# Performance work log

Hardware: AMD Instinct MI355X
Metric: run time of the kernel (lower is better)

## Reference

```python
import jax, jax.numpy as jnp
import numpy as np

D_MODEL = 768
N_HEADS = 12
HEAD_DIM = D_MODEL // N_HEADS


def setup_inputs() -> dict:
    key = jax.random.key(0)
    k_x, k_wqkv, k_bqkv, k_wp, k_bp = jax.random.split(key, 5)
    s = 1.0 / np.sqrt(D_MODEL)
    return {
        "x": jax.random.normal(k_x, (8, 1024, D_MODEL), dtype=jnp.float32),
        "w_qkv": jax.random.uniform(k_wqkv, (D_MODEL, 3 * D_MODEL), jnp.float32, -s, s),
        "b_qkv": jax.random.uniform(k_bqkv, (3 * D_MODEL,), jnp.float32, -s, s),
        "w_proj": jax.random.uniform(k_wp, (D_MODEL, D_MODEL), jnp.float32, -s, s),
        "b_proj": jax.random.uniform(k_bp, (D_MODEL,), jnp.float32, -s, s),
    }


def reference(x, w_qkv, b_qkv, w_proj, b_proj):
    # x: [B, N, D]. Dropout is identity in eval mode.
    B, N, D = x.shape
    qkv = x @ w_qkv + b_qkv  # [B, N, 3D]
    qkv = qkv.reshape(B, N, 3, N_HEADS, HEAD_DIM).transpose(2, 0, 3, 1, 4)
    q, k, v = qkv[0], qkv[1], qkv[2]  # each [B, H, N, hd]
    scale = 1.0 / np.sqrt(HEAD_DIM).astype(np.float32)
    attn = jnp.einsum("bhqd,bhkd->bhqk", q, k) * scale  # [B, H, N, N]
    attn = jax.nn.softmax(attn, axis=-1)
    out = jnp.einsum("bhqk,bhkd->bhqd", attn, v)  # [B, H, N, hd]
    out = out.transpose(0, 2, 1, 3).reshape(B, N, D)
    return out @ w_proj + b_proj
```

## Files before the change

kernel.cpp:

```cpp
#include <hip/hip_runtime.h>
#include <math.h>

#define D_MODEL 768
#define NHEADS  12
#define HDIM    64
#define SEQ     1024
#define BATCH   8
#define NBH     (BATCH*NHEADS)
#define M_TOTAL (BATCH*SEQ)
#define KT_D    (D_MODEL/32)
#define QKV_COLS (3*D_MODEL)

typedef __attribute__((ext_vector_type(8))) short bf16x8;
typedef __attribute__((ext_vector_type(4))) float f32x4;

#define MFMA16(a,b,c) __builtin_amdgcn_mfma_f32_16x16x32_bf16((a),(b),(c),0,0,0)

#define QSCALE 0.18033688011112042f

__device__ inline unsigned short f2bf(float f) {
    unsigned u = __float_as_uint(f);
    u += 0x7FFFu + ((u >> 16) & 1u);
    return (unsigned short)(u >> 16);
}
__device__ inline float bf2f(unsigned short h) {
    return __uint_as_float(((unsigned)h) << 16);
}
__device__ inline void gload16(const void* g, const void* l) {
    __builtin_amdgcn_global_load_lds(
        (const __attribute__((address_space(1))) unsigned*)g,
        (__attribute__((address_space(3))) unsigned*)l, 16, 0, 0);
}
__device__ inline float exp2_fast(float x) {
#if __has_builtin(__builtin_amdgcn_exp2f)
    return __builtin_amdgcn_exp2f(x);
#else
    float r; asm("v_exp_f32 %0, %1" : "=v"(r) : "v"(x)); return r;
#endif
}


#define NA_TOT 786432
#define NB1_TOT 221184
#define NB2_TOT 73728

__global__ __launch_bounds__(256)
void convert_all(const float* __restrict__ x,    unsigned short* __restrict__ Xf,
                 const float* __restrict__ wq,   unsigned short* __restrict__ Wq,
                 const float* __restrict__ wp,   unsigned short* __restrict__ Wp)
{
    const int gid = blockIdx.x * 256 + threadIdx.x;
    const int lane = gid & 63;
    if (gid < NA_TOT) {
        const int sub = gid >> 6;
        const int kt = sub % KT_D;
        const int mt = sub / KT_D;
        const float* s = x + (size_t)(mt*16 + (lane & 15)) * D_MODEL + kt*32 + (lane >> 4)*8;
        float4 v0 = *(const float4*)(s);
        float4 v1 = *(const float4*)(s + 4);
        float vv[8] = {v0.x, v0.y, v0.z, v0.w, v1.x, v1.y, v1.z, v1.w};
        union { unsigned short u[8]; bf16x8 v; } H;
        #pragma unroll
        for (int i = 0; i < 8; ++i) H.u[i] = f2bf(vv[i]);
        *(bf16x8*)(Xf + (size_t)sub * 512 + lane * 8) = H.v;
    } else {
        const float* src;
        unsigned short* dst;
        int sub, ldN;
        if (gid < NA_TOT + NB1_TOT) {
            src = wq; dst = Wq; ldN = QKV_COLS; sub = (gid - NA_TOT) >> 6;
        } else if (gid < NA_TOT + NB1_TOT + NB2_TOT) {
            src = wp; dst = Wp; ldN = D_MODEL; sub = (gid - NA_TOT - NB1_TOT) >> 6;
        } else {
            return;
        }
        const int kt = sub % KT_D;
        const int nt = sub / KT_D;
        const int n  = nt*16 + (lane & 15);
        const int k0 = kt*32 + (lane >> 4)*8;
        const float* s = src + (size_t)k0 * ldN + n;
        union { unsigned short u[8]; bf16x8 v; } H;
        #pragma unroll
        for (int i = 0; i < 8; ++i) H.u[i] = f2bf(s[(size_t)i * ldN]);
        *(bf16x8*)(dst + (size_t)sub * 512 + lane * 8) = H.v;
    }
}

template<int MODE>
__global__ __launch_bounds__(MODE == 0 ? 512 : 256, 4)
void gemm_frag(const unsigned short* __restrict__ Af,
               const unsigned short* __restrict__ Bf,
               const float* __restrict__ bias,
               float* __restrict__ outF,
               unsigned short* __restrict__ outQ,
               unsigned short* __restrict__ outK,
               unsigned short* __restrict__ outV)
{
    constexpr int NW     = (MODE == 0) ? 8 : 4;
    constexpr int NSUB_N = (MODE == 0) ? 8 : 4;
    constexpr int ACH    = 8;
    constexpr int NCH    = ACH + NSUB_N;
    constexpr int CPW    = NCH / NW;
    __shared__ unsigned short sm[3][NCH * 512];
    const int t = threadIdx.x, lane = t & 63, wid = t >> 6;
    const int wr = (MODE == 0) ? (wid >> 2) : (wid >> 1);
    const int wc = (MODE == 0) ? (wid & 3)  : (wid & 1);
    const int bid = blockIdx.x;
    const int mb = (bid & 7) * 8 + ((bid >> 3) & 7);
    const int nb = bid >> 6;

    auto stage = [&](int b, int ktv) {
        #pragma unroll
        for (int i = 0; i < CPW; ++i) {
            const int c = wid * CPW + i;
            const unsigned short* g;
            if (c < ACH) {
                g = Af + ((size_t)(mb*8 + c)*KT_D + ktv)*512 + lane*8;
            } else {
                const int j = c - ACH;
                g = Bf + ((size_t)(nb*NSUB_N + j)*KT_D + ktv)*512 + lane*8;
            }
            gload16(g, (const char*)&sm[b][0] + (size_t)c*1024);
        }
    };

    f32x4 acc[4][2] = {};

    stage(0, 0);
    stage(1, 1);

    for (int kt = 0; kt < KT_D; ++kt) {
        if (kt + 1 < KT_D) {
            if (MODE == 0) asm volatile("s_waitcnt vmcnt(2)" ::: "memory");
            else           asm volatile("s_waitcnt vmcnt(3)" ::: "memory");
        } else {
            asm volatile("s_waitcnt vmcnt(0)" ::: "memory");
        }
        __builtin_amdgcn_s_barrier();

        if (kt + 2 < KT_D) stage((kt + 2) % 3, kt + 2);

        const unsigned short* Lb = &sm[kt % 3][0];
        bf16x8 bh[2];
        #pragma unroll
        for (int n = 0; n < 2; ++n)
            bh[n] = *(const bf16x8*)(Lb + (ACH + wc*2 + n)*512 + lane*8);
        bf16x8 ah[4];
        #pragma unroll
        for (int m = 0; m < 4; ++m)
            ah[m] = *(const bf16x8*)(Lb + (wr*4 + m)*512 + lane*8);
        __builtin_amdgcn_s_setprio(1);
        #pragma unroll
        for (int m = 0; m < 4; ++m)
            #pragma unroll
            for (int n = 0; n < 2; ++n)
                acc[m][n] = MFMA16(ah[m], bh[n], acc[m][n]);
        __builtin_amdgcn_s_setprio(0);
    }

    const int rowW = mb*128 + wr*64;
    const int colW = nb*(NSUB_N*16) + wc*32;
    if (MODE == 1) {
        #pragma unroll
        for (int m = 0; m < 4; ++m)
            #pragma unroll
            for (int n = 0; n < 2; ++n) {
                const int col = colW + n*16 + (lane & 15);
                const float bv = bias[col];
                #pragma unroll
                for (int r = 0; r < 4; ++r) {
                    const int row = rowW + m*16 + (lane >> 4)*4 + r;
                    outF[(size_t)row * D_MODEL + col] = acc[m][n][r] + bv;
                }
            }
    } else {
        const int which = colW / D_MODEL;
        const int h     = (colW % D_MODEL) >> 6;
        #pragma unroll
        for (int m = 0; m < 4; ++m)
            #pragma unroll
            for (int n = 0; n < 2; ++n) {
                const int col = colW + n*16 + (lane & 15);
                const int d = col & 63;
                const float bv = bias[col];
                #pragma unroll
                for (int r = 0; r < 4; ++r) {
                    const int row = rowW + m*16 + (lane >> 4)*4 + r;
                    const int b = row >> 10, sq = row & 1023;
                    float val = acc[m][n][r] + bv;
                    if (which <= 1) {
                        if (which == 0) val *= QSCALE;
                        const int sub = (sq >> 4)*2 + (d >> 5);
                        const int lp  = (sq & 15) + (((d & 31) >> 3) << 4);
                        unsigned short* dst = (which == 0) ? outQ : outK;
                        dst[(size_t)(b*NHEADS + h)*65536
                            + (size_t)sub*512 + lp*8 + (d & 7)] = f2bf(val);
                    } else {
                        const int sub = (d >> 4)*32 + (sq >> 5);
                        const int lp  = (d & 15) + (((sq & 31) >> 3) << 4);
                        outV[(size_t)(b*NHEADS + h)*65536
                             + (size_t)sub*512 + lp*8 + (sq & 7)] = f2bf(val);
                    }
                }
            }
    }
}

__global__ __launch_bounds__(512, 6)
void attn_frag(const unsigned short* __restrict__ Qf,
               const unsigned short* __restrict__ Kf,
               const unsigned short* __restrict__ Vf,
               unsigned short* __restrict__ Cf)
{
    __shared__ unsigned short Ksm[2][8 * 512];
    __shared__ unsigned short Vsm[2][8 * 512];
    __shared__ unsigned short Psm[8 * 1024];

    const int t = threadIdx.x, lane = t & 63, wid = t >> 6;
    const int bid = blockIdx.x;
    const int qb  = (bid >> 3) & 7;
    const int bh  = (bid & 7) * 12 + (bid >> 6);
    const int mt0 = qb*8 + wid;
    const size_t kBase = (size_t)bh * 65536;

    const int slot  = lane & 7;
    const int colg  = (lane & 15) >> 3;
    const int qrow0 = (lane >> 4) * 4;

    auto stage = [&](int b, int jt) {
        #pragma unroll
        for (int i = 0; i < 2; ++i) {
            const int ch = wid*2 + i;
            if (ch < 8) {
                const unsigned short* gk = Kf + kBase + (size_t)(jt*8 + ch)*512;
                gload16(gk + lane*8, (const char*)&Ksm[b][0] + (size_t)ch*1024);
            } else {
                const int cv = ch - 8;
                const unsigned short* gv = Vf + kBase
                    + (size_t)((cv >> 1)*32 + jt*2 + (cv & 1))*512;
                gload16(gv + lane*8, (const char*)&Vsm[b][0] + (size_t)cv*1024);
            }
        }
    };

    stage(0, 0);

    bf16x8 qh[2];
    #pragma unroll
    for (int kt = 0; kt < 2; ++kt)
        qh[kt] = *(const bf16x8*)(Qf + kBase + ((size_t)mt0*2 + kt)*512 + lane*8);

    bf16x8 ones;
    #pragma unroll
    for (int i = 0; i < 8; ++i) ones[i] = (short)0x3F80;

    f32x4 out[4] = {};
    f32x4 lacc = {};
    float m_run[4];
    #pragma unroll
    for (int r = 0; r < 4; ++r) m_run[r] = -INFINITY;

    unsigned short* Pw = Psm + wid * 1024;

    __syncthreads();

    for (int jt = 0; jt < 16; ++jt) {
        const int cur = jt & 1;
        if (jt + 1 < 16) stage(cur ^ 1, jt + 1);

        f32x4 s[4] = {};
        __builtin_amdgcn_s_setprio(1);
        #pragma unroll
        for (int jn = 0; jn < 4; ++jn)
            #pragma unroll
            for (int kt = 0; kt < 2; ++kt) {
                const bf16x8 kh = *(const bf16x8*)(&Ksm[cur][0] + (jn*2 + kt)*512 + lane*8);
                s[jn] = MFMA16(qh[kt], kh, s[jn]);
            }
        __builtin_amdgcn_s_setprio(0);

        float mx[4];
        int ok = 1;
        #pragma unroll
        for (int r = 0; r < 4; ++r) {
            const float v = fmaxf(fmaxf(s[0][r], s[1][r]), fmaxf(s[2][r], s[3][r]));
            mx[r] = v;
            ok &= (v <= m_run[r] + 8.0f);
        }
        if (!__all(ok)) {
            float alf[4];
            #pragma unroll
            for (int r = 0; r < 4; ++r) {
                float v = mx[r];
                #pragma unroll
                for (int msk = 1; msk < 16; msk <<= 1)
                    v = fmaxf(v, __shfl_xor(v, msk));
                const float mn = fmaxf(m_run[r], v);
                alf[r] = exp2_fast(m_run[r] - mn);
                m_run[r] = mn;
            }
            #pragma unroll
            for (int dt = 0; dt < 4; ++dt)
                #pragma unroll
                for (int r = 0; r < 4; ++r)
                    out[dt][r] *= alf[r];
            #pragma unroll
            for (int r = 0; r < 4; ++r)
                lacc[r] *= alf[r];
        }

        #pragma unroll
        for (int r = 0; r < 4; ++r) {
            const float mb_ = m_run[r];
            const int tl   = qrow0 + r + (colg << 4);
            const int idxb = ((tl << 3) | slot) ^ (tl & 0x18);
            #pragma unroll
            for (int jn = 0; jn < 4; ++jn) {
                const float e = exp2_fast(s[jn][r] - mb_);
                Pw[(jn >> 1)*512 + idxb + ((jn & 1) << 8)]
                    = (unsigned short)(__float_as_uint(e) >> 16);
            }
        }

        const int rdswz = (lane*8) ^ (lane & 0x18);
        __builtin_amdgcn_s_setprio(1);
        #pragma unroll
        for (int kt2 = 0; kt2 < 2; ++kt2) {
            const bf16x8 pa = *(const bf16x8*)(Pw + kt2*512 + rdswz);
            #pragma unroll
            for (int dt = 0; dt < 4; ++dt) {
                const bf16x8 vh = *(const bf16x8*)(&Vsm[cur][0] + (dt*2 + kt2)*512 + lane*8);
                out[dt] = MFMA16(pa, vh, out[dt]);
            }
            lacc = MFMA16(pa, ones, lacc);
        }
        __builtin_amdgcn_s_setprio(0);

        __syncthreads();
    }

    const int b = bh / NHEADS, h = bh % NHEADS;
    #pragma unroll
    for (int r = 0; r < 4; ++r) {
        const float inv = 1.0f / lacc[r];
        const int sq = mt0*16 + qrow0 + r;
        const int mrow = b*SEQ + sq;
        #pragma unroll
        for (int dt = 0; dt < 4; ++dt) {
            const int c = h*64 + dt*16 + (lane & 15);
            const float val = out[dt][r] * inv;
            Cf[((size_t)(mrow >> 4)*KT_D + (c >> 5))*512
               + ((mrow & 15) + (((c & 31) >> 3) << 4))*8 + (c & 7)] = f2bf(val);
        }
    }
}

extern "C" void kernel_launch(void* const* d_in, const int* in_sizes, int n_in,
                              void* d_out, int out_size, void* d_ws, size_t ws_size,
                              hipStream_t stream)
{
    const float* x      = (const float*)d_in[0];
    const float* w_qkv  = (const float*)d_in[1];
    const float* b_qkv  = (const float*)d_in[2];
    const float* w_proj = (const float*)d_in[3];
    const float* b_proj = (const float*)d_in[4];
    float* out = (float*)d_out;

    unsigned short* ws = (unsigned short*)d_ws;
    unsigned short* Xf = ws;
    unsigned short* Wq = Xf + 6291456;
    unsigned short* Wp = Wq + 1769472;
    unsigned short* Qf = Wp + 589824;
    unsigned short* Kf = Qf + 6291456;
    unsigned short* Vf = Kf + 6291456;
    unsigned short* Cf = Vf + 6291456;

    convert_all<<<dim3(4224), 256, 0, stream>>>(x, Xf, w_qkv, Wq, w_proj, Wp);

    gemm_frag<0><<<dim3(1152), 512, 0, stream>>>(Xf, Wq, b_qkv, nullptr, Qf, Kf, Vf);
    attn_frag<<<dim3(768), 512, 0, stream>>>(Qf, Kf, Vf, Cf);
    gemm_frag<1><<<dim3(768), 256, 0, stream>>>(Cf, Wp, b_proj, out,
                                                nullptr, nullptr, nullptr);
}
```

Before: 112.5 us.

## Give each attention wave two query tiles and unroll GEMM ring by three

The attention kernel now runs 4 waves per block, each handling two 16-row query tiles. Every K/V fragment loaded from LDS feeds two MFMAs, which halves LDS reads per FLOP, and the softmax and P staging are duplicated per tile. The GEMM main loop is unrolled by three so triple-buffer indices are compile-time constants, removing the modulo buffer addressing. The cost is higher register pressure and fewer waves per block for the attention kernel, which could reduce latency hiding.

Measured after the change: 124.8 us. 1.11x slower.

```diff
diff --git a/kernel.cpp b/kernel.cpp
--- a/kernel.cpp
+++ b/kernel.cpp
@@ -22,9 +22,6 @@
     unsigned u = __float_as_uint(f);
     u += 0x7FFFu + ((u >> 16) & 1u);
     return (unsigned short)(u >> 16);
-}
-__device__ inline float bf2f(unsigned short h) {
-    return __uint_as_float(((unsigned)h) << 16);
 }
 __device__ inline void gload16(const void* g, const void* l) {
     __builtin_amdgcn_global_load_lds(
@@ -109,7 +106,9 @@
     const int mb = (bid & 7) * 8 + ((bid >> 3) & 7);
     const int nb = bid >> 6;
 
-    auto stage = [&](int b, int ktv) {
+    f32x4 acc[4][2] = {};
+
+    auto stageTo = [&](unsigned short* Lb, int ktv) {
         #pragma unroll
         for (int i = 0; i < CPW; ++i) {
             const int c = wid * CPW + i;
@@ -120,27 +119,14 @@
                 const int j = c - ACH;
                 g = Bf + ((size_t)(nb*NSUB_N + j)*KT_D + ktv)*512 + lane*8;
             }
-            gload16(g, (const char*)&sm[b][0] + (size_t)c*1024);
+            gload16(g, (const char*)Lb + (size_t)c*1024);
         }
     };
-
-    f32x4 acc[4][2] = {};
-
-    stage(0, 0);
-    stage(1, 1);
-
-    for (int kt = 0; kt < KT_D; ++kt) {
-        if (kt + 1 < KT_D) {
-            if (MODE == 0) asm volatile("s_waitcnt vmcnt(2)" ::: "memory");
-            else           asm volatile("s_waitcnt vmcnt(3)" ::: "memory");
-        } else {
-            asm volatile("s_waitcnt vmcnt(0)" ::: "memory");
-        }
-        __builtin_amdgcn_s_barrier();
-
-        if (kt + 2 < KT_D) stage((kt + 2) % 3, kt + 2);
-
-        const unsigned short* Lb = &sm[kt % 3][0];
+    auto waitCPW = [&] {
+        if (MODE == 0) asm volatile("s_waitcnt vmcnt(2)" ::: "memory");
+        else           asm volatile("s_waitcnt vmcnt(3)" ::: "memory");
+    };
+    auto compute = [&](const unsigned short* Lb) {
         bf16x8 bh[2];
         #pragma unroll
         for (int n = 0; n < 2; ++n)
@@ -156,7 +142,26 @@
             for (int n = 0; n < 2; ++n)
                 acc[m][n] = MFMA16(ah[m], bh[n], acc[m][n]);
         __builtin_amdgcn_s_setprio(0);
+    };
+
+    stageTo(&sm[0][0], 0);
+    stageTo(&sm[1][0], 1);
+
+    for (int ktb = 0; ktb < KT_D - 3; ktb += 3) {
+        waitCPW(); __builtin_amdgcn_s_barrier();
+        stageTo(&sm[2][0], ktb + 2);  compute(&sm[0][0]);
+        waitCPW(); __builtin_amdgcn_s_barrier();
+        stageTo(&sm[0][0], ktb + 3);  compute(&sm[1][0]);
+        waitCPW(); __builtin_amdgcn_s_barrier();
+        stageTo(&sm[1][0], ktb + 4);  compute(&sm[2][0]);
     }
+    waitCPW(); __builtin_amdgcn_s_barrier();
+    stageTo(&sm[2][0], KT_D - 1);  compute(&sm[0][0]);
+    waitCPW(); __builtin_amdgcn_s_barrier();
+    compute(&sm[1][0]);
+    asm volatile("s_waitcnt vmcnt(0)" ::: "memory");
+    __builtin_amdgcn_s_barrier();
+    compute(&sm[2][0]);
 
     const int rowW = mb*128 + wr*64;
     const int colW = nb*(NSUB_N*16) + wc*32;
@@ -206,7 +211,7 @@
     }
 }
 
-__global__ __launch_bounds__(512, 6)
+__global__ __launch_bounds__(256, 3)
 void attn_frag(const unsigned short* __restrict__ Qf,
                const unsigned short* __restrict__ Kf,
                const unsigned short* __restrict__ Vf,
@@ -214,13 +219,13 @@
 {
     __shared__ unsigned short Ksm[2][8 * 512];
     __shared__ unsigned short Vsm[2][8 * 512];
-    __shared__ unsigned short Psm[8 * 1024];
+    __shared__ unsigned short Psm[4 * 2048];
 
     const int t = threadIdx.x, lane = t & 63, wid = t >> 6;
     const int bid = blockIdx.x;
     const int qb  = (bid >> 3) & 7;
     const int bh  = (bid & 7) * 12 + (bid >> 6);
-    const int mt0 = qb*8 + wid;
+    const int mt0 = qb*8 + wid*2;
     const size_t kBase = (size_t)bh * 65536;
 
     const int slot  = lane & 7;
@@ -229,8 +234,8 @@
 
     auto stage = [&](int b, int jt) {
         #pragma unroll
-        for (int i = 0; i < 2; ++i) {
-            const int ch = wid*2 + i;
+        for (int i = 0; i < 4; ++i) {
+            const int ch = wid*4 + i;
             if (ch < 8) {
                 const unsigned short* gk = Kf + kBase + (size_t)(jt*8 + ch)*512;
                 gload16(gk + lane*8, (const char*)&Ksm[b][0] + (size_t)ch*1024);
@@ -245,22 +250,27 @@
 
     stage(0, 0);
 
-    bf16x8 qh[2];
+    bf16x8 qh[2][2];
     #pragma unroll
-    for (int kt = 0; kt < 2; ++kt)
-        qh[kt] = *(const bf16x8*)(Qf + kBase + ((size_t)mt0*2 + kt)*512 + lane*8);
+    for (int m = 0; m < 2; ++m)
+        #pragma unroll
+        for (int kt = 0; kt < 2; ++kt)
+            qh[m][kt] = *(const bf16x8*)(Qf + kBase
+                            + ((size_t)(mt0 + m)*2 + kt)*512 + lane*8);
 
     bf16x8 ones;
     #pragma unroll
     for (int i = 0; i < 8; ++i) ones[i] = (short)0x3F80;
 
-    f32x4 out[4] = {};
-    f32x4 lacc = {};
-    float m_run[4];
+    f32x4 out[2][4] = {};
+    f32x4 lacc[2] = {};
+    float m_run[2][4];
     #pragma unroll
-    for (int r = 0; r < 4; ++r) m_run[r] = -INFINITY;
-
-    unsigned short* Pw = Psm + wid * 1024;
+    for (int m = 0; m < 2; ++m)
+        #pragma unroll
+        for (int r = 0; r < 4; ++r) m_run[m][r] = -INFINITY;
+
+    unsigned short* Pw = Psm + wid * 2048;
 
     __syncthreads();
 
@@ -268,71 +278,90 @@
         const int cur = jt & 1;
         if (jt + 1 < 16) stage(cur ^ 1, jt + 1);
 
-        f32x4 s[4] = {};
+        f32x4 s[2][4] = {};
         __builtin_amdgcn_s_setprio(1);
         #pragma unroll
         for (int jn = 0; jn < 4; ++jn)
             #pragma unroll
             for (int kt = 0; kt < 2; ++kt) {
                 const bf16x8 kh = *(const bf16x8*)(&Ksm[cur][0] + (jn*2 + kt)*512 + lane*8);
-                s[jn] = MFMA16(qh[kt], kh, s[jn]);
+                #pragma unroll
+                for (int m = 0; m < 2; ++m)
+                    s[m][jn] = MFMA16(qh[m][kt], kh, s[m][jn]);
             }
         __builtin_amdgcn_s_setprio(0);
 
-        float mx[4];
+        float mx[2][4];
         int ok = 1;
         #pragma unroll
-        for (int r = 0; r < 4; ++r) {
-            const float v = fmaxf(fmaxf(s[0][r], s[1][r]), fmaxf(s[2][r], s[3][r]));
-            mx[r] = v;
-            ok &= (v <= m_run[r] + 8.0f);
-        }
+        for (int m = 0; m < 2; ++m)
+            #pragma unroll
+            for (int r = 0; r < 4; ++r) {
+                const float v = fmaxf(fmaxf(s[m][0][r], s[m][1][r]),
+                                      fmaxf(s[m][2][r], s[m][3][r]));
+                mx[m][r] = v;
+                ok &= (v <= m_run[m][r] + 8.0f);
+            }
         if (!__all(ok)) {
-            float alf[4];
+            float alf[2][4];
+            #pragma unroll
+            for (int m = 0; m < 2; ++m)
+                #pragma unroll
+                for (int r = 0; r < 4; ++r) {
+                    float v = mx[m][r];
+                    #pragma unroll
+                    for (int msk = 1; msk < 16; msk <<= 1)
+                        v = fmaxf(v, __shfl_xor(v, msk));
+                    const float mn = fmaxf(m_run[m][r], v);
+                    alf[m][r] = exp2_fast(m_run[m][r] - mn);
+                    m_run[m][r] = mn;
+                }
+            #pragma unroll
+            for (int m = 0; m < 2; ++m) {
+                #pragma unroll
+                for (int dt = 0; dt < 4; ++dt)
+                    #pragma unroll
+                    for (int r = 0; r < 4; ++r)
+                        out[m][dt][r] *= alf[m][r];
+                #pragma unroll
+                for (int r = 0; r < 4; ++r)
+                    lacc[m][r] *= alf[m][r];
+            }
+        }
+
+        #pragma unroll
+        for (int m = 0; m < 2; ++m)
             #pragma unroll
             for (int r = 0; r < 4; ++r) {
-                float v = mx[r];
-                #pragma unroll
-                for (int msk = 1; msk < 16; msk <<= 1)
-                    v = fmaxf(v, __shfl_xor(v, msk));
-                const float mn = fmaxf(m_run[r], v);
-                alf[r] = exp2_fast(m_run[r] - mn);
-                m_run[r] = mn;
-            }
-            #pragma unroll
-            for (int dt = 0; dt < 4; ++dt)
-                #pragma unroll
-                for (int r = 0; r < 4; ++r)
-                    out[dt][r] *= alf[r];
-            #pragma unroll
-            for (int r = 0; r < 4; ++r)
-                lacc[r] *= alf[r];
-        }
-
-        #pragma unroll
-        for (int r = 0; r < 4; ++r) {
-            const float mb_ = m_run[r];
-            const int tl   = qrow0 + r + (colg << 4);
-            const int idxb = ((tl << 3) | slot) ^ (tl & 0x18);
-            #pragma unroll
-            for (int jn = 0; jn < 4; ++jn) {
-                const float e = exp2_fast(s[jn][r] - mb_);
-                Pw[(jn >> 1)*512 + idxb + ((jn & 1) << 8)]
-                    = (unsigned short)(__float_as_uint(e) >> 16);
-            }
-        }
+                const float mb_ = m_run[m][r];
+                const int tl   = qrow0 + r + (colg << 4);
+                const int idxb = ((tl << 3) | slot) ^ (tl & 0x18);
+                #pragma unroll
+                for (int jn = 0; jn < 4; ++jn) {
+                    const float e = exp2_fast(s[m][jn][r] - mb_);
+                    Pw[(m*2 + (jn >> 1))*512 + idxb + ((jn & 1) << 8)]
+                        = (unsigned short)(__float_as_uint(e) >> 16);
+                }
+            }
 
         const int rdswz = (lane*8) ^ (lane & 0x18);
         __builtin_amdgcn_s_setprio(1);
         #pragma unroll
         for (int kt2 = 0; kt2 < 2; ++kt2) {
-            const bf16x8 pa = *(const bf16x8*)(Pw + kt2*512 + rdswz);
+            bf16x8 pa[2];
+            #pragma unroll
+            for (int m = 0; m < 2; ++m)
+                pa[m] = *(const bf16x8*)(Pw + (m*2 + kt2)*512 + rdswz);
             #pragma unroll
             for (int dt = 0; dt < 4; ++dt) {
                 const bf16x8 vh = *(const bf16x8*)(&Vsm[cur][0] + (dt*2 + kt2)*512 + lane*8);
-                out[dt] = MFMA16(pa, vh, out[dt]);
-            }
-            lacc = MFMA16(pa, ones, lacc);
+                #pragma unroll
+                for (int m = 0; m < 2; ++m)
+                    out[m][dt] = MFMA16(pa[m], vh, out[m][dt]);
+            }
+            #pragma unroll
+            for (int m = 0; m < 2; ++m)
+                lacc[m] = MFMA16(pa[m], ones, lacc[m]);
         }
         __builtin_amdgcn_s_setprio(0);
 
@@ -341,18 +370,20 @@
 
     const int b = bh / NHEADS, h = bh % NHEADS;
     #pragma unroll
-    for (int r = 0; r < 4; ++r) {
-        const float inv = 1.0f / lacc[r];
-        const int sq = mt0*16 + qrow0 + r;
-        const int mrow = b*SEQ + sq;
-        #pragma unroll
-        for (int dt = 0; dt < 4; ++dt) {
-            const int c = h*64 + dt*16 + (lane & 15);
-            const float val = out[dt][r] * inv;
-            Cf[((size_t)(mrow >> 4)*KT_D + (c >> 5))*512
-               + ((mrow & 15) + (((c & 31) >> 3) << 4))*8 + (c & 7)] = f2bf(val);
-        }
-    }
+    for (int m = 0; m < 2; ++m)
+        #pragma unroll
+        for (int r = 0; r < 4; ++r) {
+            const float inv = 1.0f / lacc[m][r];
+            const int sq = (mt0 + m)*16 + qrow0 + r;
+            const int mrow = b*SEQ + sq;
+            #pragma unroll
+            for (int dt = 0; dt < 4; ++dt) {
+                const int c = h*64 + dt*16 + (lane & 15);
+                const float val = out[m][dt][r] * inv;
+                Cf[((size_t)(mrow >> 4)*KT_D + (c >> 5))*512
+                   + ((mrow & 15) + (((c & 31) >> 3) << 4))*8 + (c & 7)] = f2bf(val);
+            }
+        }
 }
 
 extern "C" void kernel_launch(void* const* d_in, const int* in_sizes, int n_in,
@@ -378,7 +409,7 @@
     convert_all<<<dim3(4224), 256, 0, stream>>>(x, Xf, w_qkv, Wq, w_proj, Wp);
 
     gemm_frag<0><<<dim3(1152), 512, 0, stream>>>(Xf, Wq, b_qkv, nullptr, Qf, Kf, Vf);
-    attn_frag<<<dim3(768), 512, 0, stream>>>(Qf, Kf, Vf, Cf);
+    attn_frag<<<dim3(768), 256, 0, stream>>>(Qf, Kf, Vf, Cf);
     gemm_frag<1><<<dim3(768), 256, 0, stream>>>(Cf, Wp, b_proj, out,
                                                 nullptr, nullptr, nullptr);
 }
```
